# Optimization experiments

Hardware: AMD Instinct MI355X
Metric: run time of the kernel (lower is better)

Reference implementation:

```python
import jax, jax.numpy as jnp
import numpy as np

N, E = 10000, 160000
MUL0, MUL1, MUL2 = 64, 32, 16
DIM = MUL0 + MUL1 * 3 + MUL2 * 5          # 240
LAT, CPL, NTYPE = 128, 128, 95
NGATE = MUL1 + MUL2                        # 48 gate scalars
NCH = MUL0 + MUL1 + MUL2                   # 112 irrep channels
AVG_NEI = 16.0

# scaling_indices: per-channel index repeated over each irrep's dim
SCALE_IDX = np.concatenate([
    np.arange(MUL0),
    np.repeat(np.arange(MUL0, MUL0 + MUL1), 3),
    np.repeat(np.arange(MUL0 + MUL1, NCH), 5),
])


def _split(x, n):
    s = x[:, :MUL0]
    v1 = x[:, MUL0:MUL0 + MUL1 * 3].reshape(n, MUL1, 3)
    v2 = x[:, MUL0 + MUL1 * 3:].reshape(n, MUL2, 5)
    return s, v1, v2


def setup_inputs() -> dict:
    key = jax.random.key(0)
    ks = iter(jax.random.split(key, 48))
    rn = lambda *s: jax.random.normal(next(ks), s, dtype=jnp.float32)
    return dict(
        node_features=rn(N, DIM), edge_features=rn(E, DIM),
        latents=rn(E, LAT), msg_cpl=rn(N, CPL),
        node_onehot=jax.random.uniform(next(ks), (N, NTYPE), dtype=jnp.float32),
        wigner_D1=rn(E, 3, 3), wigner_D2=rn(E, 5, 5),
        so2_W0=rn(2 * MUL0, MUL0 + NGATE) * 0.08, so2_W1=rn(2 * MUL1, MUL1) * 0.12,
        so2_W2=rn(2 * MUL2, MUL2) * 0.17, so2_Ws=rn(LAT, NCH + NGATE) * 0.08,
        env_W=rn(LAT, NCH) * 0.08,
        post_W0=rn(MUL0, MUL0) * 0.12, post_b0=rn(MUL0) * 0.01,
        post_W1=rn(MUL1, MUL1) * 0.17, post_W2=rn(MUL2, MUL2) * 0.25,
        res_W0=rn(MUL0, MUL0) * 0.12, res_b0=rn(MUL0) * 0.01,
        res_W1=rn(MUL1, MUL1) * 0.17, res_W2=rn(MUL2, MUL2) * 0.25,
        cpl_W1=rn(CPL, CPL) * 0.08, cpl_b1=rn(CPL) * 0.01,
        cpl_W2=rn(CPL, NCH) * 0.08, cpl_b2=rn(NCH) * 0.01,
        gs_W=rn(MUL0, CPL) * 0.12, gs_b=rn(CPL) * 0.01,
        msg_W1=rn(2 * CPL, CPL) * 0.06, msg_b1=rn(CPL) * 0.01,
        msg_W2=rn(CPL, CPL) * 0.08, msg_b2=rn(CPL) * 0.01,
        ln_g=jnp.ones(CPL, jnp.float32), ln_b=jnp.zeros(CPL, jnp.float32),
        oh_w0=rn(MUL0, NTYPE) * 0.1, oh_w1=rn(MUL1, NTYPE) * 0.1, oh_w2=rn(MUL2, NTYPE) * 0.1,
        edge_index=jax.random.randint(next(ks), (2, E), 0, N),
    )


def _forward(node_features, edge_features, latents, msg_cpl, node_onehot,
             wigner_D1, wigner_D2, so2_W0, so2_W1, so2_W2, so2_Ws, env_W,
             post_W0, post_b0, post_W1, post_W2, res_W0, res_b0, res_W1, res_W2,
             cpl_W1, cpl_b1, cpl_W2, cpl_b2, gs_W, gs_b,
             msg_W1, msg_b1, msg_W2, msg_b2, ln_g, ln_b,
             oh_w0, oh_w1, oh_w2, edge_index):
    src = edge_index[0]
    ns, nv1, nv2 = _split(node_features, N)
    es, ev1, ev2 = _split(edge_features, E)
    # gather node feats to edges, concat with edge feats (per-l blocks)
    s_in = jnp.concatenate([ns[src], es], axis=1)                 # [E,128]
    v1_in = jnp.concatenate([nv1[src], ev1], axis=1)              # [E,64,3]
    v2_in = jnp.concatenate([nv2[src], ev2], axis=1)              # [E,32,5]
    # rotate into per-edge frame (Wigner D)
    v1_r = jnp.einsum('eij,ecj->eci', wigner_D1, v1_in)
    v2_r = jnp.einsum('eij,ecj->eci', wigner_D2, v2_in)
    # SO2 linear: shared channel mixing + latent-conditioned per-channel scales
    sc = latents @ so2_Ws                                         # [E,160]
    s_m = (s_in @ so2_W0) * sc[:, :MUL0 + NGATE]
    v1_m = jnp.einsum('eci,co->eoi', v1_r, so2_W1) * sc[:, MUL0 + NGATE:MUL0 + NGATE + MUL1, None]
    v2_m = jnp.einsum('eci,co->eoi', v2_r, so2_W2) * sc[:, MUL0 + NGATE + MUL1:, None]
    # rotate back
    v1_m = jnp.einsum('eji,eci->ecj', wigner_D1, v1_m)
    v2_m = jnp.einsum('eji,eci->ecj', wigner_D2, v2_m)
    # Gate activation
    s_act = jax.nn.silu(s_m[:, :MUL0])
    gates = jax.nn.sigmoid(s_m[:, MUL0:])
    v1_g = v1_m * gates[:, :MUL1, None]
    v2_g = v2_m * gates[:, MUL1:, None]
    # lin_post (per-l linear, bias on scalars)
    s_p = s_act @ post_W0 + post_b0
    v1_p = jnp.einsum('eci,co->eoi', v1_g, post_W1)
    v2_p = jnp.einsum('eci,co->eoi', v2_g, post_W2)
    # env element-wise weighting from latents
    w = latents @ env_W                                           # [E,112]
    s_p = s_p * w[:, :MUL0]
    v1_p = v1_p * w[:, MUL0:MUL0 + MUL1, None]
    v2_p = v2_p * w[:, MUL0 + MUL1:, None]
    msg = jnp.concatenate([s_p, v1_p.reshape(E, -1), v2_p.reshape(E, -1)], axis=1)
    # scatter-reduce to nodes + neighbor normalization
    agg = jax.ops.segment_sum(msg, src, num_segments=N) * (AVG_NEI ** -0.5)
    # coupling coefficients (per-channel, expanded by scaling_indices)
    coeffs = jax.nn.silu(msg_cpl @ cpl_W1 + cpl_b1) @ cpl_W2 + cpl_b2
    new_nf = agg * coeffs[:, SCALE_IDX]
    # coupling-channel update
    scal = new_nf[:, :MUL0] @ gs_W + gs_b
    h = jnp.concatenate([scal, msg_cpl], axis=1)
    upd = jax.nn.silu(h @ msg_W1 + msg_b1) @ msg_W2 + msg_b2
    mc = msg_cpl + upd
    mu = mc.mean(-1, keepdims=True)
    var = mc.var(-1, keepdims=True)
    msg_cpl_out = (mc - mu) * jax.lax.rsqrt(var + 1e-5) * ln_g + ln_b
    # residual mix with fixed logit-0 coefficients
    c = jax.nn.sigmoid(jnp.float32(0.0))
    c_old = jax.lax.rsqrt(c * c + 1.0)
    c_new = c * c_old
    rs = ns @ res_W0 + res_b0
    rv1 = jnp.einsum('eci,co->eoi', nv1, res_W1)
    rv2 = jnp.einsum('eci,co->eoi', nv2, res_W2)
    res = jnp.concatenate([rs, rv1.reshape(N, -1), rv2.reshape(N, -1)], axis=1)
    nf = c_new * new_nf + c_old * res
    # layer one-hot tensor product ('uvu' with 95x0e)
    inv = 1.0 / np.sqrt(NTYPE).astype(np.float32)
    g0 = (node_onehot @ oh_w0.T) * inv
    g1 = (node_onehot @ oh_w1.T) * inv
    g2 = (node_onehot @ oh_w2.T) * inv
    os_, ov1, ov2 = _split(nf, N)
    oh = jnp.concatenate([os_ * g0, (ov1 * g1[:, :, None]).reshape(N, -1),
                          (ov2 * g2[:, :, None]).reshape(N, -1)], axis=1)
    return nf + oh, msg_cpl_out


def reference(node_features, edge_features, latents, msg_cpl, node_onehot,
              wigner_D1, wigner_D2, so2_W0, so2_W1, so2_W2, so2_Ws, env_W,
              post_W0, post_b0, post_W1, post_W2, res_W0, res_b0, res_W1, res_W2,
              cpl_W1, cpl_b1, cpl_W2, cpl_b2, gs_W, gs_b,
              msg_W1, msg_b1, msg_W2, msg_b2, ln_g, ln_b,
              oh_w0, oh_w1, oh_w2, edge_index):
    return _forward(node_features, edge_features, latents, msg_cpl, node_onehot,
                    wigner_D1, wigner_D2, so2_W0, so2_W1, so2_W2, so2_Ws, env_W,
                    post_W0, post_b0, post_W1, post_W2, res_W0, res_b0, res_W1, res_W2,
                    cpl_W1, cpl_b1, cpl_W2, cpl_b2, gs_W, gs_b,
                    msg_W1, msg_b1, msg_W2, msg_b2, ln_g, ln_b,
                    oh_w0, oh_w1, oh_w2, edge_index)
```

## Files before the change

kernel.cpp:

```cpp
#include <hip/hip_runtime.h>

#define NN   10000
#define NE   160000
#define DIM  240
#define EB   16
#define NPB  16

typedef __bf16 bf16x8 __attribute__((ext_vector_type(8)));
typedef __bf16 bf16x4 __attribute__((ext_vector_type(4)));
typedef float  f32x4  __attribute__((ext_vector_type(4)));

__device__ __forceinline__ float sigf(float x) { return 1.0f / (1.0f + __expf(-x)); }

#define OFF_WB1 0
#define OFF_WB2 34816
#define OFF_W1  49152
#define OFF_W2  51200
#define OFF_PW0 51712
#define OFF_PW1 55808
#define OFF_PW2 56832
#define OHT_BYTE_OFF 131072
#define CNT_BYTE_OFF 196608
#define ROW_BYTE_OFF 237568
#define CUR_BYTE_OFF 282624
#define EID_BYTE_OFF 327680
#define MSG_BYTE_OFF 1048576

__global__ __launch_bounds__(256) void prep_kernel(
    const float* __restrict__ Ws, const float* __restrict__ We, const float* __restrict__ W0,
    const float* __restrict__ W1, const float* __restrict__ W2,
    const float* __restrict__ pW0, const float* __restrict__ pW1, const float* __restrict__ pW2,
    const float* __restrict__ w0g, const float* __restrict__ w1g, const float* __restrict__ w2g,
    __bf16* __restrict__ wsb, float* __restrict__ ohT)
{
    int tid = blockIdx.x * 256 + threadIdx.x;
    int stride = gridDim.x * 256;
    for (int idx = tid; idx < 17*4*512; idx += stride) {
        int j = idx & 7, lane = (idx >> 3) & 63, ks = (idx >> 9) & 3, nt = idx >> 11;
        int k = ks*32 + (lane >> 4)*8 + j, n = nt*16 + (lane & 15);
        float v = (n < 160) ? Ws[k*160 + n] : We[k*112 + (n - 160)];
        wsb[OFF_WB1 + idx] = (__bf16)v;
    }
    for (int idx = tid; idx < 7*4*512; idx += stride) {
        int j = idx & 7, lane = (idx >> 3) & 63, ks = (idx >> 9) & 3, nt = idx >> 11;
        int k = ks*32 + (lane >> 4)*8 + j, n = nt*16 + (lane & 15);
        wsb[OFF_WB2 + idx] = (__bf16)W0[k*112 + n];
    }
    for (int idx = tid; idx < 2*2*512; idx += stride) {
        int j = idx & 7, lane = (idx >> 3) & 63, ks = (idx >> 9) & 1, nt = idx >> 10;
        int k = ks*32 + (lane >> 4)*8 + j, n = nt*16 + (lane & 15);
        wsb[OFF_W1 + idx] = (__bf16)W1[k*32 + n];
    }
    for (int idx = tid; idx < 512; idx += stride) {
        int j = idx & 7, lane = (idx >> 3) & 63;
        int k = (lane >> 4)*8 + j, n = lane & 15;
        wsb[OFF_W2 + idx] = (__bf16)W2[k*16 + n];
    }
    for (int idx = tid; idx < 4*2*512; idx += stride) {
        int j = idx & 7, lane = (idx >> 3) & 63, ks = (idx >> 9) & 1, nt = idx >> 10;
        int k = ks*32 + (lane >> 4)*8 + j, n = nt*16 + (lane & 15);
        wsb[OFF_PW0 + idx] = (__bf16)pW0[k*64 + n];
    }
    for (int idx = tid; idx < 2*512; idx += stride) {
        int j = idx & 7, lane = (idx >> 3) & 63, nt = idx >> 9;
        int k = (lane >> 4)*8 + j, n = nt*16 + (lane & 15);
        wsb[OFF_PW1 + idx] = (__bf16)pW1[k*32 + n];
    }
    for (int idx = tid; idx < 512; idx += stride) {
        int j = idx & 7, lane = (idx >> 3) & 63;
        int k = (lane >> 4)*8 + j, n = lane & 15;
        wsb[OFF_PW2 + idx] = (k < 16) ? (__bf16)pW2[k*16 + n] : (__bf16)0.0f;
    }
    for (int idx = tid; idx < 96*112; idx += stride) {
        int k = idx / 112, n2 = idx - k*112;
        float v = 0.f;
        if (k < 95) {
            if (n2 < 64)      v = w0g[n2*95 + k];
            else if (n2 < 96) v = w1g[(n2-64)*95 + k];
            else              v = w2g[(n2-96)*95 + k];
        }
        ohT[idx] = v * 0.10259783521f;
    }
}

__global__ __launch_bounds__(256) void count_kernel(const int* __restrict__ src, int* __restrict__ cnt) {
    int e = blockIdx.x * 256 + threadIdx.x;
    if (e < NE) atomicAdd(&cnt[src[e]], 1);
}

__global__ __launch_bounds__(256) void scan_kernel(const int* __restrict__ cnt,
                                                   int* __restrict__ rowptr, int* __restrict__ cur) {
    __shared__ int part[256];
    int t = threadIdx.x;
    int base = t * 40;
    int local[40];
    int s = 0;
    #pragma unroll
    for (int i = 0; i < 40; i++) {
        int idx = base + i;
        int v = (idx < NN) ? cnt[idx] : 0;
        local[i] = s; s += v;
    }
    part[t] = s;
    __syncthreads();
    for (int off = 1; off < 256; off <<= 1) {
        int v = (t >= off) ? part[t - off] : 0;
        __syncthreads();
        part[t] += v;
        __syncthreads();
    }
    int pre = (t > 0) ? part[t - 1] : 0;
    #pragma unroll
    for (int i = 0; i < 40; i++) {
        int idx = base + i;
        if (idx < NN) { int r = pre + local[i]; rowptr[idx] = r; cur[idx] = r; }
    }
    if (t == 255) rowptr[NN] = part[255];
}

__global__ __launch_bounds__(256) void fill_kernel(const int* __restrict__ src,
                                                   int* __restrict__ cur, int* __restrict__ eidl) {
    int e = blockIdx.x * 256 + threadIdx.x;
    if (e < NE) {
        int slot = atomicAdd(&cur[src[e]], 1);
        eidl[slot] = e;
    }
}

__global__ __launch_bounds__(256) void agg_kernel(
    const __bf16* __restrict__ msg, const int* __restrict__ rowptr,
    const int* __restrict__ eidl, float* __restrict__ out0)
{
    int wid = threadIdx.x >> 6, lane = threadIdx.x & 63;
    int node = blockIdx.x * 4 + wid;
    if (node >= NN || lane >= 60) return;
    int beg = rowptr[node], end = rowptr[node + 1];
    float a0 = 0.f, a1 = 0.f, a2 = 0.f, a3 = 0.f;
    int i = beg;
    for (; i + 4 <= end; i += 4) {
        int e0 = eidl[i], e1 = eidl[i+1], e2 = eidl[i+2], e3 = eidl[i+3];
        bf16x4 v0 = *(const bf16x4*)(msg + (size_t)e0*240 + lane*4);
        bf16x4 v1 = *(const bf16x4*)(msg + (size_t)e1*240 + lane*4);
        bf16x4 v2 = *(const bf16x4*)(msg + (size_t)e2*240 + lane*4);
        bf16x4 v3 = *(const bf16x4*)(msg + (size_t)e3*240 + lane*4);
        a0 += (float)v0[0] + (float)v1[0] + (float)v2[0] + (float)v3[0];
        a1 += (float)v0[1] + (float)v1[1] + (float)v2[1] + (float)v3[1];
        a2 += (float)v0[2] + (float)v1[2] + (float)v2[2] + (float)v3[2];
        a3 += (float)v0[3] + (float)v1[3] + (float)v2[3] + (float)v3[3];
    }
    for (; i < end; i++) {
        int e = eidl[i];
        bf16x4 v = *(const bf16x4*)(msg + (size_t)e*240 + lane*4);
        a0 += (float)v[0]; a1 += (float)v[1]; a2 += (float)v[2]; a3 += (float)v[3];
    }
    float4 r = { a0, a1, a2, a3 };
    *(float4*)(out0 + (size_t)node*240 + lane*4) = r;
}

__global__ __launch_bounds__(256, 4) void edge_mfma_kernel(
    const float* __restrict__ nf, const float* __restrict__ ef,
    const float* __restrict__ latg, const float* __restrict__ D1g, const float* __restrict__ D2g,
    const float* __restrict__ pb0, const int* __restrict__ srcg,
    const __bf16* __restrict__ wsb, float* agg, __bf16* __restrict__ msgout)
{
    __shared__ __align__(16) unsigned char pool[37376];
    __bf16* Cb   = (__bf16*)(pool + 0);
    __bf16* vst  = (__bf16*)(pool + 0);
    __bf16* aLat = (__bf16*)(pool + 12544);
    __bf16* aSin = (__bf16*)(pool + 16640);
    __bf16* v1m  = (__bf16*)(pool + 12544);
    __bf16* v2m  = (__bf16*)(pool + 15712);
    __bf16* aV1r = (__bf16*)(pool + 20736);
    __bf16* aV2r = (__bf16*)(pool + 26880);
    __bf16* aSact= (__bf16*)(pool + 20736);
    __bf16* aV1g = (__bf16*)(pool + 22784);
    __bf16* aV2g = (__bf16*)(pool + 25856);
    float*  d1s  = (float*)(pool + 32000);
    float*  d2s  = (float*)(pool + 32576);
    float*  gts  = (float*)(pool + 34176);
    int*    srcs = (int*)  (pool + 37312);

    const int t    = threadIdx.x;
    const int wid  = t >> 6, lane = t & 63;
    const int e0   = blockIdx.x * EB;

    if (t < 16) srcs[t] = srcg[e0 + t];
    __syncthreads();

    for (int idx = t; idx < 144; idx += 256) d1s[idx] = D1g[e0*9  + idx];
    for (int idx = t; idx < 400; idx += 256) d2s[idx] = D2g[e0*25 + idx];
    for (int idx = t; idx < 16*88; idx += 256) {
        int e = idx / 88, c4 = idx - e*88;
        const float4* p = (c4 < 44) ? (const float4*)(nf + srcs[e]*240 + 64 + c4*4)
                                    : (const float4*)(ef + (e0 + e)*240 + 64 + (c4 - 44)*4);
        float4 f = *p;
        bf16x4 v = { (__bf16)f.x, (__bf16)f.y, (__bf16)f.z, (__bf16)f.w };
        *(bf16x4*)(vst + e*360 + c4*4) = v;
    }
    {
        int ks = t >> 6, l2 = t & 63, e = l2 & 15, q = l2 >> 4;
        int k0 = ks*32 + q*8;
        {
            const float4* p4 = (const float4*)(latg + (e0 + e)*128 + k0);
            float4 f0 = p4[0], f1 = p4[1];
            bf16x8 v;
            v[0]=(__bf16)f0.x; v[1]=(__bf16)f0.y; v[2]=(__bf16)f0.z; v[3]=(__bf16)f0.w;
            v[4]=(__bf16)f1.x; v[5]=(__bf16)f1.y; v[6]=(__bf16)f1.z; v[7]=(__bf16)f1.w;
            *(bf16x8*)(aLat + t*8) = v;
        }
        {
            const float* s2 = (k0 < 64) ? (nf + srcs[e]*240 + k0)
                                        : (ef + (e0 + e)*240 + (k0 - 64));
            const float4* p4 = (const float4*)s2;
            float4 f0 = p4[0], f1 = p4[1];
            bf16x8 v;
            v[0]=(__bf16)f0.x; v[1]=(__bf16)f0.y; v[2]=(__bf16)f0.z; v[3]=(__bf16)f0.w;
            v[4]=(__bf16)f1.x; v[5]=(__bf16)f1.y; v[6]=(__bf16)f1.z; v[7]=(__bf16)f1.w;
            *(bf16x8*)(aSin + t*8) = v;
        }
    }
    __syncthreads();

    for (int idx = t; idx < 384; idx += 256) {
        int i = idx >> 7, rem = idx & 127, ks = rem >> 6, l2 = rem & 63;
        int e = l2 & 15, q = l2 >> 4;
        int c0 = ks*32 + q*8;
        float da = d1s[e*9 + i*3 + 0], db = d1s[e*9 + i*3 + 1], dc = d1s[e*9 + i*3 + 2];
        const __bf16* ve = vst + e*360;
        bf16x8 v;
        #pragma unroll
        for (int j = 0; j < 8; j++) {
            int c = c0 + j;
            const __bf16* p = (c < 32) ? (ve + c*3) : (ve + 176 + (c - 32)*3);
            v[j] = (__bf16)(da*(float)p[0] + db*(float)p[1] + dc*(float)p[2]);
        }
        *(bf16x8*)(aV1r + idx*8) = v;
    }
    for (int idx = t; idx < 320; idx += 256) {
        int i = idx >> 6, l2 = idx & 63, e = l2 & 15, q = l2 >> 4;
        int c0 = q*8;
        const float* dd = d2s + e*25 + i*5;
        const __bf16* ve = vst + e*360;
        bf16x8 v;
        #pragma unroll
        for (int j = 0; j < 8; j++) {
            int c = c0 + j;
            const __bf16* p = (c < 16) ? (ve + 96 + c*5) : (ve + 272 + (c - 16)*5);
            float a = 0.f;
            #pragma unroll
            for (int z = 0; z < 5; z++) a += dd[z]*(float)p[z];
            v[j] = (__bf16)a;
        }
        *(bf16x8*)(aV2r + idx*8) = v;
    }
    __syncthreads();

    {
        int col16 = lane & 15, ebase = (lane >> 4)*4;
        bf16x8 aL[4], aS[4];
        #pragma unroll
        for (int ks = 0; ks < 4; ks++) {
            aL[ks] = *(const bf16x8*)(aLat + (ks*64 + lane)*8);
            aS[ks] = *(const bf16x8*)(aSin + (ks*64 + lane)*8);
        }
        #pragma unroll
        for (int it = 0; it < 6; it++) {
            int nt = wid + it*4;
            bool isLat = nt < 17;
            const __bf16* bB = isLat ? (wsb + OFF_WB1 + nt*2048)
                                     : (wsb + OFF_WB2 + (nt - 17)*2048);
            f32x4 acc = {0.f, 0.f, 0.f, 0.f};
            #pragma unroll
            for (int ks = 0; ks < 4; ks++) {
                bf16x8 b = *(const bf16x8*)(bB + (ks*64 + lane)*8);
                acc = __builtin_amdgcn_mfma_f32_16x16x32_bf16(isLat ? aL[ks] : aS[ks], b, acc, 0, 0, 0);
            }
            int col = (isLat ? nt*16 : 272 + (nt - 17)*16) + col16;
            #pragma unroll
            for (int r = 0; r < 4; r++) Cb[(ebase + r)*392 + col] = (__bf16)acc[r];
        }
    }
    __syncthreads();

    {
        int col16 = lane & 15, ebase = (lane >> 4)*4;
        for (int p = wid; p < 11; p += 4) {
            f32x4 acc = {0.f, 0.f, 0.f, 0.f};
            if (p < 6) {
                int i = p >> 1, nt = p & 1;
                #pragma unroll
                for (int ks = 0; ks < 2; ks++) {
                    bf16x8 a = *(const bf16x8*)(aV1r + ((i*2 + ks)*64 + lane)*8);
                    bf16x8 b = *(const bf16x8*)(wsb + OFF_W1 + ((nt*2 + ks)*64 + lane)*8);
                    acc = __builtin_amdgcn_mfma_f32_16x16x32_bf16(a, b, acc, 0, 0, 0);
                }
                int col = nt*16 + col16;
                #pragma unroll
                for (int r = 0; r < 4; r++) v1m[(i*16 + ebase + r)*33 + col] = (__bf16)acc[r];
            } else {
                int i = p - 6;
                bf16x8 a = *(const bf16x8*)(aV2r + (i*64 + lane)*8);
                bf16x8 b = *(const bf16x8*)(wsb + OFF_W2 + lane*8);
                acc = __builtin_amdgcn_mfma_f32_16x16x32_bf16(a, b, acc, 0, 0, 0);
                #pragma unroll
                for (int r = 0; r < 4; r++) v2m[(i*16 + ebase + r)*17 + col16] = (__bf16)acc[r];
            }
        }
    }
    __syncthreads();

    if (t < 128) {
        int ks = t >> 6, l2 = t & 63, e = l2 & 15, o0 = ks*32 + (l2 >> 4)*8;
        bf16x8 v;
        #pragma unroll
        for (int j = 0; j < 8; j++) {
            int o = o0 + j;
            float x = (float)Cb[e*392 + 272 + o] * (float)Cb[e*392 + o];
            v[j] = (__bf16)(x * sigf(x));
        }
        *(bf16x8*)(aSact + t*8) = v;
    }
    for (int idx = t; idx < 768; idx += 256) {
        int e = idx / 48, o = idx - e*48;
        float x = (float)Cb[e*392 + 336 + o] * (float)Cb[e*392 + 64 + o];
        gts[e*49 + o] = sigf(x);
    }
    __syncthreads();

    for (int idx = t; idx < 512; idx += 256) {
        if (idx < 192) {
            int i = idx >> 6, l2 = idx & 63, e = l2 & 15, c0 = (l2 >> 4)*8;
            float d0 = d1s[e*9 + i*3], d1 = d1s[e*9 + i*3 + 1], d2 = d1s[e*9 + i*3 + 2];
            bf16x8 v;
            #pragma unroll
            for (int j = 0; j < 8; j++) {
                int c = c0 + j;
                float scl = (float)Cb[e*392 + 112 + c];
                float g   = gts[e*49 + c];
                float m0 = (float)v1m[e*33 + c], m1 = (float)v1m[(16 + e)*33 + c],
                      m2 = (float)v1m[(32 + e)*33 + c];
                v[j] = (__bf16)(g * scl * (d0*m0 + d1*m1 + d2*m2));
            }
            *(bf16x8*)(aV1g + idx*8) = v;
        } else {
            int idx2 = idx - 192;
            int i = idx2 >> 6, l2 = idx2 & 63, e = l2 & 15, c0 = (l2 >> 4)*8;
            const float* dd = d2s + e*25 + i*5;
            bf16x8 v;
            #pragma unroll
            for (int j = 0; j < 8; j++) {
                int c = c0 + j;
                float val = 0.f;
                if (c < 16) {
                    float scl = (float)Cb[e*392 + 144 + c];
                    float g   = gts[e*49 + 32 + c];
                    float acc = 0.f;
                    #pragma unroll
                    for (int z = 0; z < 5; z++) acc += dd[z] * (float)v2m[(z*16 + e)*17 + c];
                    val = g * scl * acc;
                }
                v[j] = (__bf16)val;
            }
            *(bf16x8*)(aV2g + idx2*8) = v;
        }
    }
    __syncthreads();

    {
        int col16 = lane & 15, ebase = (lane >> 4)*4;
        for (int p = wid; p < 15; p += 4) {
            f32x4 acc = {0.f, 0.f, 0.f, 0.f};
            if (p < 4) {
                int nt = p;
                #pragma unroll
                for (int ks = 0; ks < 2; ks++) {
                    bf16x8 a = *(const bf16x8*)(aSact + (ks*64 + lane)*8);
                    bf16x8 b = *(const bf16x8*)(wsb + OFF_PW0 + ((nt*2 + ks)*64 + lane)*8);
                    acc = __builtin_amdgcn_mfma_f32_16x16x32_bf16(a, b, acc, 0, 0, 0);
                }
                int o = nt*16 + col16;
                float bias = pb0[o];
                #pragma unroll
                for (int r = 0; r < 4; r++) {
                    int e = ebase + r;
                    float val = (acc[r] + bias) * (float)Cb[e*392 + 160 + o];
                    if (msgout) msgout[(size_t)(e0 + e)*240 + o] = (__bf16)val;
                    else        atomicAdd(agg + srcs[e]*240 + o, val);
                }
            } else if (p < 10) {
                int q = p - 4, i = q >> 1, nt = q & 1;
                bf16x8 a = *(const bf16x8*)(aV1g + (i*64 + lane)*8);
                bf16x8 b = *(const bf16x8*)(wsb + OFF_PW1 + (nt*64 + lane)*8);
                acc = __builtin_amdgcn_mfma_f32_16x16x32_bf16(a, b, acc, 0, 0, 0);
                int o = nt*16 + col16;
                #pragma unroll
                for (int r = 0; r < 4; r++) {
                    int e = ebase + r;
                    float val = acc[r] * (float)Cb[e*392 + 224 + o];
                    if (msgout) msgout[(size_t)(e0 + e)*240 + 64 + o*3 + i] = (__bf16)val;
                    else        atomicAdd(agg + srcs[e]*240 + 64 + o*3 + i, val);
                }
            } else {
                int i = p - 10;
                bf16x8 a = *(const bf16x8*)(aV2g + (i*64 + lane)*8);
                bf16x8 b = *(const bf16x8*)(wsb + OFF_PW2 + lane*8);
                acc = __builtin_amdgcn_mfma_f32_16x16x32_bf16(a, b, acc, 0, 0, 0);
                #pragma unroll
                for (int r = 0; r < 4; r++) {
                    int e = ebase + r;
                    float val = acc[r] * (float)Cb[e*392 + 256 + col16];
                    if (msgout) msgout[(size_t)(e0 + e)*240 + 160 + col16*5 + i] = (__bf16)val;
                    else        atomicAdd(agg + srcs[e]*240 + 160 + col16*5 + i, val);
                }
            }
        }
    }
}

__global__ __launch_bounds__(256, 2) void node_kernel(
    const float* __restrict__ nf, const float* __restrict__ mcplg,
    const float* __restrict__ ohg,
    const float* __restrict__ cW1, const float* __restrict__ cb1,
    const float* __restrict__ cW2, const float* __restrict__ cb2,
    const float* __restrict__ gsW, const float* __restrict__ gsb,
    const float* __restrict__ mW1, const float* __restrict__ mb1,
    const float* __restrict__ mW2, const float* __restrict__ mb2,
    const float* __restrict__ lng, const float* __restrict__ lnb,
    const float* __restrict__ rW0, const float* __restrict__ rb0,
    const float* __restrict__ rW1, const float* __restrict__ rW2,
    const float* __restrict__ ohT, float* out0, float* out1)
{
    __shared__ __align__(16) unsigned char pool[68608];
    float* mcp  = (float*)(pool + 0);
    float* ohv  = (float*)(pool + 8192);
    float* nsr  = (float*)(pool + 14336);
    float* anew = (float*)(pool + 29696);
    float* t12  = (float*)(pool + 45056);
    float* cfg  = (float*)(pool + 53248);
    float* scm  = (float*)(pool + 60416);

    const int t  = threadIdx.x;
    const int g  = t >> 7;
    const int o  = t & 127;
    const int nb = g * 8;
    const int n0 = blockIdx.x * NPB;

    for (int idx = t; idx < NPB * 128; idx += 256) {
        int n = idx >> 7, k = idx & 127;
        mcp[n*128 + k] = mcplg[(n0 + n) * 128 + k];
    }
    for (int idx = t; idx < NPB * 96; idx += 256) {
        int n = idx / 96, k = idx - n * 96;
        ohv[n*96 + k] = (k < 95) ? ohg[(n0 + n) * 95 + k] : 0.f;
    }
    for (int idx = t; idx < NPB * 240; idx += 256) {
        int n = idx / 240, k = idx - n * 240;
        nsr[n*240 + k]  = nf[(n0 + n) * DIM + k];
        anew[n*240 + k] = out0[(n0 + n) * DIM + k];
    }
    __syncthreads();

    {
        float a[8]; float b = cb1[o];
        #pragma unroll
        for (int i = 0; i < 8; i++) a[i] = b;
        #pragma unroll 2
        for (int k4 = 0; k4 < 32; k4++) {
            float w0 = cW1[(4*k4+0)*128 + o], w1 = cW1[(4*k4+1)*128 + o],
                  w2 = cW1[(4*k4+2)*128 + o], w3 = cW1[(4*k4+3)*128 + o];
            #pragma unroll
            for (int i = 0; i < 8; i++) {
                float4 m = *(const float4*)&mcp[(nb+i)*128 + 4*k4];
                a[i] += m.x*w0 + m.y*w1 + m.z*w2 + m.w*w3;
            }
        }
        #pragma unroll
        for (int i = 0; i < 8; i++) { float x = a[i]; t12[(nb+i)*128 + o] = x * sigf(x); }
    }
    __syncthreads();

    if (o < 112) {
        float a[8]; float b = cb2[o];
        #pragma unroll
        for (int i = 0; i < 8; i++) a[i] = b;
        #pragma unroll 2
        for (int k4 = 0; k4 < 32; k4++) {
            float w0 = cW2[(4*k4+0)*112 + o], w1 = cW2[(4*k4+1)*112 + o],
                  w2 = cW2[(4*k4+2)*112 + o], w3 = cW2[(4*k4+3)*112 + o];
            #pragma unroll
            for (int i = 0; i < 8; i++) {
                float4 m = *(const float4*)&t12[(nb+i)*128 + 4*k4];
                a[i] += m.x*w0 + m.y*w1 + m.z*w2 + m.w*w3;
            }
        }
        #pragma unroll
        for (int i = 0; i < 8; i++) cfg[(nb+i)*112 + o] = a[i];
    }
    __syncthreads();

    for (int idx = t; idx < NPB * 240; idx += 256) {
        int n = idx / 240, d = idx - n * 240;
        int ch = (d < 64) ? d : (d < 160 ? 64 + (d - 64) / 3 : 96 + (d - 160) / 5);
        anew[n*240 + d] *= 0.25f * cfg[n*112 + ch];
    }
    __syncthreads();

    {
        float a[8]; float b = gsb[o];
        #pragma unroll
        for (int i = 0; i < 8; i++) a[i] = b;
        #pragma unroll 2
        for (int k4 = 0; k4 < 16; k4++) {
            float w0 = gsW[(4*k4+0)*128 + o], w1 = gsW[(4*k4+1)*128 + o],
                  w2 = gsW[(4*k4+2)*128 + o], w3 = gsW[(4*k4+3)*128 + o];
            #pragma unroll
            for (int i = 0; i < 8; i++) {
                float4 m = *(const float4*)&anew[(nb+i)*240 + 4*k4];
                a[i] += m.x*w0 + m.y*w1 + m.z*w2 + m.w*w3;
            }
        }
        #pragma unroll
        for (int i = 0; i < 8; i++) scm[(nb+i)*128 + o] = a[i];
    }
    __syncthreads();

    {
        float a[8]; float b = mb1[o];
        #pragma unroll
        for (int i = 0; i < 8; i++) a[i] = b;
        #pragma unroll 2
        for (int k4 = 0; k4 < 32; k4++) {
            float w0 = mW1[(4*k4+0)*128 + o], w1 = mW1[(4*k4+1)*128 + o],
                  w2 = mW1[(4*k4+2)*128 + o], w3 = mW1[(4*k4+3)*128 + o];
            #pragma unroll
            for (int i = 0; i < 8; i++) {
                float4 m = *(const float4*)&scm[(nb+i)*128 + 4*k4];
                a[i] += m.x*w0 + m.y*w1 + m.z*w2 + m.w*w3;
            }
        }
        #pragma unroll 2
        for (int k4 = 0; k4 < 32; k4++) {
            float w0 = mW1[(128+4*k4+0)*128 + o], w1 = mW1[(128+4*k4+1)*128 + o],
                  w2 = mW1[(128+4*k4+2)*128 + o], w3 = mW1[(128+4*k4+3)*128 + o];
            #pragma unroll
            for (int i = 0; i < 8; i++) {
                float4 m = *(const float4*)&mcp[(nb+i)*128 + 4*k4];
                a[i] += m.x*w0 + m.y*w1 + m.z*w2 + m.w*w3;
            }
        }
        #pragma unroll
        for (int i = 0; i < 8; i++) { float x = a[i]; t12[(nb+i)*128 + o] = x * sigf(x); }
    }
    __syncthreads();

    {
        float a[8]; float b = mb2[o];
        #pragma unroll
        for (int i = 0; i < 8; i++) a[i] = b;
        #pragma unroll 2
        for (int k4 = 0; k4 < 32; k4++) {
            float w0 = mW2[(4*k4+0)*128 + o], w1 = mW2[(4*k4+1)*128 + o],
                  w2 = mW2[(4*k4+2)*128 + o], w3 = mW2[(4*k4+3)*128 + o];
            #pragma unroll
            for (int i = 0; i < 8; i++) {
                float4 m = *(const float4*)&t12[(nb+i)*128 + 4*k4];
                a[i] += m.x*w0 + m.y*w1 + m.z*w2 + m.w*w3;
            }
        }
        #pragma unroll
        for (int i = 0; i < 8; i++) scm[(nb+i)*128 + o] = mcp[(nb+i)*128 + o] + a[i];
    }
    __syncthreads();

    {
        int n = t >> 4, l = t & 15;
        float x[8]; float s = 0.f, ss = 0.f;
        #pragma unroll
        for (int i = 0; i < 8; i++) { x[i] = scm[n*128 + l + 16*i]; s += x[i]; ss += x[i]*x[i]; }
        #pragma unroll
        for (int off = 8; off > 0; off >>= 1) {
            s  += __shfl_down(s,  off, 16);
            ss += __shfl_down(ss, off, 16);
        }
        s  = __shfl(s, 0, 16);
        ss = __shfl(ss, 0, 16);
        float mu   = s * (1.f / 128.f);
        float var  = ss * (1.f / 128.f) - mu * mu;
        float rstd = rsqrtf(var + 1e-5f);
        float* op = out1 + (n0 + n) * 128;
        #pragma unroll
        for (int i = 0; i < 8; i++) {
            int c = l + 16*i;
            op[c] = (x[i] - mu) * rstd * lng[c] + lnb[c];
        }
    }

    if (o < 112) {
        float a[8] = {0.f,0.f,0.f,0.f,0.f,0.f,0.f,0.f};
        #pragma unroll 2
        for (int k4 = 0; k4 < 24; k4++) {
            float w0 = ohT[(4*k4+0)*112 + o], w1 = ohT[(4*k4+1)*112 + o],
                  w2 = ohT[(4*k4+2)*112 + o], w3 = ohT[(4*k4+3)*112 + o];
            #pragma unroll
            for (int i = 0; i < 8; i++) {
                float4 m = *(const float4*)&ohv[(nb+i)*96 + 4*k4];
                a[i] += m.x*w0 + m.y*w1 + m.z*w2 + m.w*w3;
            }
        }
        #pragma unroll
        for (int i = 0; i < 8; i++) cfg[(nb+i)*112 + o] = a[i];
    }
    __syncthreads();

    const float c_new = 0.4472135955f;
    const float c_old = 0.8944271910f;
    for (int idx = t; idx < NPB * 240; idx += 256) {
        int n = idx / 240, d = idx - n * 240;
        float res, gg;
        if (d < 64) {
            float acc = rb0[d];
            #pragma unroll 4
            for (int c = 0; c < 64; c++) acc += nsr[n*240 + c] * rW0[c * 64 + d];
            res = acc; gg = cfg[n*112 + d];
        } else if (d < 160) {
            int dd = d - 64, oo = dd / 3, j = dd - oo * 3;
            float acc = 0.f;
            #pragma unroll 4
            for (int c = 0; c < 32; c++) acc += nsr[n*240 + 64 + c*3 + j] * rW1[c * 32 + oo];
            res = acc; gg = cfg[n*112 + 64 + oo];
        } else {
            int dd = d - 160, oo = dd / 5, j = dd - oo * 5;
            float acc = 0.f;
            #pragma unroll 4
            for (int c = 0; c < 16; c++) acc += nsr[n*240 + 160 + c*5 + j] * rW2[c * 16 + oo];
            res = acc; gg = cfg[n*112 + 96 + oo];
        }
        float v = c_new * anew[n*240 + d] + c_old * res;
        out0[(n0 + n) * DIM + d] = v * (1.f + gg);
    }
}

extern "C" void kernel_launch(void* const* d_in, const int* in_sizes, int n_in,
                              void* d_out, int out_size, void* d_ws, size_t ws_size,
                              hipStream_t stream) {
    const float* nf      = (const float*)d_in[0];
    const float* ef      = (const float*)d_in[1];
    const float* lat     = (const float*)d_in[2];
    const float* mcpl    = (const float*)d_in[3];
    const float* ohot    = (const float*)d_in[4];
    const float* D1      = (const float*)d_in[5];
    const float* D2      = (const float*)d_in[6];
    const float* so2_W0  = (const float*)d_in[7];
    const float* so2_W1  = (const float*)d_in[8];
    const float* so2_W2  = (const float*)d_in[9];
    const float* so2_Ws  = (const float*)d_in[10];
    const float* env_W   = (const float*)d_in[11];
    const float* post_W0 = (const float*)d_in[12];
    const float* post_b0 = (const float*)d_in[13];
    const float* post_W1 = (const float*)d_in[14];
    const float* post_W2 = (const float*)d_in[15];
    const float* res_W0  = (const float*)d_in[16];
    const float* res_b0  = (const float*)d_in[17];
    const float* res_W1  = (const float*)d_in[18];
    const float* res_W2  = (const float*)d_in[19];
    const float* cpl_W1  = (const float*)d_in[20];
    const float* cpl_b1  = (const float*)d_in[21];
    const float* cpl_W2  = (const float*)d_in[22];
    const float* cpl_b2  = (const float*)d_in[23];
    const float* gs_W    = (const float*)d_in[24];
    const float* gs_b    = (const float*)d_in[25];
    const float* msg_W1  = (const float*)d_in[26];
    const float* msg_b1  = (const float*)d_in[27];
    const float* msg_W2  = (const float*)d_in[28];
    const float* msg_b2  = (const float*)d_in[29];
    const float* ln_g    = (const float*)d_in[30];
    const float* ln_b    = (const float*)d_in[31];
    const float* oh_w0   = (const float*)d_in[32];
    const float* oh_w1   = (const float*)d_in[33];
    const float* oh_w2   = (const float*)d_in[34];
    const int*   eidx    = (const int*)d_in[35];

    float* out0 = (float*)d_out;
    float* out1 = (float*)d_out + (size_t)NN * DIM;
    char*   wsB = (char*)d_ws;
    __bf16* wsb = (__bf16*)d_ws;
    float*  ohT = (float*)(wsB + OHT_BYTE_OFF);

    const size_t need = (size_t)MSG_BYTE_OFF + (size_t)NE * 240 * 2;
    const bool planA = ws_size >= need;

    (void)hipMemsetAsync(out0, 0, (size_t)NN * DIM * sizeof(float), stream);

    prep_kernel<<<56, 256, 0, stream>>>(so2_Ws, env_W, so2_W0, so2_W1, so2_W2,
                                        post_W0, post_W1, post_W2,
                                        oh_w0, oh_w1, oh_w2, wsb, ohT);

    if (planA) {
        int*    cnt  = (int*)(wsB + CNT_BYTE_OFF);
        int*    row  = (int*)(wsB + ROW_BYTE_OFF);
        int*    cur  = (int*)(wsB + CUR_BYTE_OFF);
        int*    eidl = (int*)(wsB + EID_BYTE_OFF);
        __bf16* msg  = (__bf16*)(wsB + MSG_BYTE_OFF);

        (void)hipMemsetAsync(cnt, 0, 10240 * sizeof(int), stream);
        count_kernel<<<(NE + 255) / 256, 256, 0, stream>>>(eidx, cnt);
        scan_kernel<<<1, 256, 0, stream>>>(cnt, row, cur);
        fill_kernel<<<(NE + 255) / 256, 256, 0, stream>>>(eidx, cur, eidl);

        edge_mfma_kernel<<<NE / EB, 256, 0, stream>>>(
            nf, ef, lat, D1, D2, post_b0, eidx, wsb, out0, msg);

        agg_kernel<<<(NN + 3) / 4, 256, 0, stream>>>(msg, row, eidl, out0);
    } else {
        edge_mfma_kernel<<<NE / EB, 256, 0, stream>>>(
            nf, ef, lat, D1, D2, post_b0, eidx, wsb, out0, nullptr);
    }

    node_kernel<<<NN / NPB, 256, 0, stream>>>(
        nf, mcpl, ohot, cpl_W1, cpl_b1, cpl_W2, cpl_b2, gs_W, gs_b,
        msg_W1, msg_b1, msg_W2, msg_b2, ln_g, ln_b,
        res_W0, res_b0, res_W1, res_W2, ohT, out0, out1);
}
```

Before: 749.6 us.

## Fold forward and inverse Wigner rotations into precomputed D·D products

Drops the separate rotate-into-frame pass over the l=1/l=2 features. The SO(2) matmuls now read features directly from transposed LDS tiles, and the back-rotation uses precomputed per-edge D·D products (e1s/e2s) in place of D itself. This removes one LDS staging pass and two barriers, and the srcs preload barrier is replaced by direct global index reads. It only matches the original if rotating before the channel-mixing matmul commutes with it, which holds because the mixing is linear per component. It also changes where bf16 rounding happens and relies on padded LDS strides (40 and 24) to avoid bank conflicts.

```diff
diff --git a/kernel.cpp b/kernel.cpp
--- a/kernel.cpp
+++ b/kernel.cpp
@@ -163,45 +163,68 @@
     const float* __restrict__ pb0, const int* __restrict__ srcg,
     const __bf16* __restrict__ wsb, float* agg, __bf16* __restrict__ msgout)
 {
-    __shared__ __align__(16) unsigned char pool[37376];
+    __shared__ __align__(16) unsigned char pool[39936];
     __bf16* Cb   = (__bf16*)(pool + 0);
-    __bf16* vst  = (__bf16*)(pool + 0);
     __bf16* aLat = (__bf16*)(pool + 12544);
     __bf16* aSin = (__bf16*)(pool + 16640);
     __bf16* v1m  = (__bf16*)(pool + 12544);
-    __bf16* v2m  = (__bf16*)(pool + 15712);
-    __bf16* aV1r = (__bf16*)(pool + 20736);
-    __bf16* aV2r = (__bf16*)(pool + 26880);
-    __bf16* aSact= (__bf16*)(pool + 20736);
-    __bf16* aV1g = (__bf16*)(pool + 22784);
-    __bf16* aV2g = (__bf16*)(pool + 25856);
-    float*  d1s  = (float*)(pool + 32000);
-    float*  d2s  = (float*)(pool + 32576);
-    float*  gts  = (float*)(pool + 34176);
-    int*    srcs = (int*)  (pool + 37312);
+    __bf16* v2m  = (__bf16*)(pool + 16384);
+    __bf16* vt1  = (__bf16*)(pool + 20736);
+    __bf16* vt2  = (__bf16*)(pool + 27136);
+    __bf16* aV1g = (__bf16*)(pool + 20736);
+    __bf16* aV2g = (__bf16*)(pool + 23808);
+    float*  d1s  = (float*)(pool + 32512);
+    float*  d2s  = (float*)(pool + 33088);
+    float*  gts  = (float*)(pool + 32512);
+    __bf16* aSact= (__bf16*)(pool + 35648);
+    float*  e1s  = (float*)(pool + 37696);
+    float*  e2s  = (float*)(pool + 38272);
 
     const int t    = threadIdx.x;
     const int wid  = t >> 6, lane = t & 63;
     const int e0   = blockIdx.x * EB;
 
-    if (t < 16) srcs[t] = srcg[e0 + t];
-    __syncthreads();
-
     for (int idx = t; idx < 144; idx += 256) d1s[idx] = D1g[e0*9  + idx];
     for (int idx = t; idx < 400; idx += 256) d2s[idx] = D2g[e0*25 + idx];
-    for (int idx = t; idx < 16*88; idx += 256) {
-        int e = idx / 88, c4 = idx - e*88;
-        const float4* p = (c4 < 44) ? (const float4*)(nf + srcs[e]*240 + 64 + c4*4)
-                                    : (const float4*)(ef + (e0 + e)*240 + 64 + (c4 - 44)*4);
-        float4 f = *p;
-        bf16x4 v = { (__bf16)f.x, (__bf16)f.y, (__bf16)f.z, (__bf16)f.w };
-        *(bf16x4*)(vst + e*360 + c4*4) = v;
-    }
-    {
-        int ks = t >> 6, l2 = t & 63, e = l2 & 15, q = l2 >> 4;
-        int k0 = ks*32 + q*8;
+    {
+        int e = t >> 4, half = (t >> 3) & 1, cq = t & 7;
+        const float* base = half ? (ef + (size_t)(e0 + e)*240 + 64 + cq*12)
+                                 : (nf + (size_t)srcg[e0 + e]*240 + 64 + cq*12);
+        float4 f0 = *(const float4*)base;
+        float4 f1 = *(const float4*)(base + 4);
+        float4 f2 = *(const float4*)(base + 8);
+        float f[12] = {f0.x,f0.y,f0.z,f0.w,f1.x,f1.y,f1.z,f1.w,f2.x,f2.y,f2.z,f2.w};
+        int c = half*32 + cq*4;
+        __bf16* dst = vt1 + e*200 + c;
+        #pragma unroll
+        for (int i = 0; i < 3; i++) {
+            bf16x4 v = {(__bf16)f[i], (__bf16)f[3+i], (__bf16)f[6+i], (__bf16)f[9+i]};
+            *(bf16x4*)(dst + i*64) = v;
+        }
+    }
+    if (t < 128) {
+        int e = t >> 3, half = (t >> 2) & 1, cq = t & 3;
+        const float* base = half ? (ef + (size_t)(e0 + e)*240 + 160 + cq*20)
+                                 : (nf + (size_t)srcg[e0 + e]*240 + 160 + cq*20);
+        float f[20];
+        #pragma unroll
+        for (int k = 0; k < 5; k++) {
+            float4 q4 = *(const float4*)(base + k*4);
+            f[4*k] = q4.x; f[4*k+1] = q4.y; f[4*k+2] = q4.z; f[4*k+3] = q4.w;
+        }
+        int c = half*16 + cq*4;
+        __bf16* dst = vt2 + e*168 + c;
+        #pragma unroll
+        for (int z = 0; z < 5; z++) {
+            bf16x4 v = {(__bf16)f[z], (__bf16)f[5+z], (__bf16)f[10+z], (__bf16)f[15+z]};
+            *(bf16x4*)(dst + z*32) = v;
+        }
+    }
+    {
+        int ks = t >> 6, l2 = t & 63, e = l2 & 15;
+        int k0 = ks*32 + (l2 >> 4)*8;
         {
-            const float4* p4 = (const float4*)(latg + (e0 + e)*128 + k0);
+            const float4* p4 = (const float4*)(latg + (size_t)(e0 + e)*128 + k0);
             float4 f0 = p4[0], f1 = p4[1];
             bf16x8 v;
             v[0]=(__bf16)f0.x; v[1]=(__bf16)f0.y; v[2]=(__bf16)f0.z; v[3]=(__bf16)f0.w;
@@ -209,8 +232,8 @@
             *(bf16x8*)(aLat + t*8) = v;
         }
         {
-            const float* s2 = (k0 < 64) ? (nf + srcs[e]*240 + k0)
-                                        : (ef + (e0 + e)*240 + (k0 - 64));
+            const float* s2 = (k0 < 64) ? (nf + (size_t)srcg[e0 + e]*240 + k0)
+                                        : (ef + (size_t)(e0 + e)*240 + (k0 - 64));
             const float4* p4 = (const float4*)s2;
             float4 f0 = p4[0], f1 = p4[1];
             bf16x8 v;
@@ -221,40 +244,6 @@
     }
     __syncthreads();
 
-    for (int idx = t; idx < 384; idx += 256) {
-        int i = idx >> 7, rem = idx & 127, ks = rem >> 6, l2 = rem & 63;
-        int e = l2 & 15, q = l2 >> 4;
-        int c0 = ks*32 + q*8;
-        float da = d1s[e*9 + i*3 + 0], db = d1s[e*9 + i*3 + 1], dc = d1s[e*9 + i*3 + 2];
-        const __bf16* ve = vst + e*360;
-        bf16x8 v;
-        #pragma unroll
-        for (int j = 0; j < 8; j++) {
-            int c = c0 + j;
-            const __bf16* p = (c < 32) ? (ve + c*3) : (ve + 176 + (c - 32)*3);
-            v[j] = (__bf16)(da*(float)p[0] + db*(float)p[1] + dc*(float)p[2]);
-        }
-        *(bf16x8*)(aV1r + idx*8) = v;
-    }
-    for (int idx = t; idx < 320; idx += 256) {
-        int i = idx >> 6, l2 = idx & 63, e = l2 & 15, q = l2 >> 4;
-        int c0 = q*8;
-        const float* dd = d2s + e*25 + i*5;
-        const __bf16* ve = vst + e*360;
-        bf16x8 v;
-        #pragma unroll
-        for (int j = 0; j < 8; j++) {
-            int c = c0 + j;
-            const __bf16* p = (c < 16) ? (ve + 96 + c*5) : (ve + 272 + (c - 16)*5);
-            float a = 0.f;
-            #pragma unroll
-            for (int z = 0; z < 5; z++) a += dd[z]*(float)p[z];
-            v[j] = (__bf16)a;
-        }
-        *(bf16x8*)(aV2r + idx*8) = v;
-    }
-    __syncthreads();
-
     {
         int col16 = lane & 15, ebase = (lane >> 4)*4;
         bf16x8 aL[4], aS[4];
@@ -280,35 +269,48 @@
             for (int r = 0; r < 4; r++) Cb[(ebase + r)*392 + col] = (__bf16)acc[r];
         }
     }
-    __syncthreads();
-
-    {
-        int col16 = lane & 15, ebase = (lane >> 4)*4;
+    for (int idx = t; idx < 544; idx += 256) {
+        if (idx < 144) {
+            int e = idx / 9, r = idx - e*9, i = r / 3, k = r - i*3;
+            const float* d = d1s + e*9;
+            e1s[idx] = d[i*3+0]*d[0*3+k] + d[i*3+1]*d[1*3+k] + d[i*3+2]*d[2*3+k];
+        } else {
+            int j = idx - 144;
+            int e = j / 25, r = j - e*25, i = r / 5, k = r - i*5;
+            const float* d = d2s + e*25;
+            float a = 0.f;
+            #pragma unroll
+            for (int tt = 0; tt < 5; tt++) a += d[i*5+tt] * d[tt*5+k];
+            e2s[j] = a;
+        }
+    }
+    __syncthreads();
+
+    {
+        int col16 = lane & 15, er = lane & 15, q8 = (lane >> 4)*8, ebase = (lane >> 4)*4;
         for (int p = wid; p < 11; p += 4) {
             f32x4 acc = {0.f, 0.f, 0.f, 0.f};
             if (p < 6) {
                 int i = p >> 1, nt = p & 1;
                 #pragma unroll
                 for (int ks = 0; ks < 2; ks++) {
-                    bf16x8 a = *(const bf16x8*)(aV1r + ((i*2 + ks)*64 + lane)*8);
+                    bf16x8 a = *(const bf16x8*)(vt1 + er*200 + i*64 + ks*32 + q8);
                     bf16x8 b = *(const bf16x8*)(wsb + OFF_W1 + ((nt*2 + ks)*64 + lane)*8);
                     acc = __builtin_amdgcn_mfma_f32_16x16x32_bf16(a, b, acc, 0, 0, 0);
                 }
                 int col = nt*16 + col16;
                 #pragma unroll
-                for (int r = 0; r < 4; r++) v1m[(i*16 + ebase + r)*33 + col] = (__bf16)acc[r];
+                for (int r = 0; r < 4; r++) v1m[(i*16 + ebase + r)*40 + col] = (__bf16)acc[r];
             } else {
                 int i = p - 6;
-                bf16x8 a = *(const bf16x8*)(aV2r + (i*64 + lane)*8);
+                bf16x8 a = *(const bf16x8*)(vt2 + er*168 + i*32 + q8);
                 bf16x8 b = *(const bf16x8*)(wsb + OFF_W2 + lane*8);
                 acc = __builtin_amdgcn_mfma_f32_16x16x32_bf16(a, b, acc, 0, 0, 0);
                 #pragma unroll
-                for (int r = 0; r < 4; r++) v2m[(i*16 + ebase + r)*17 + col16] = (__bf16)acc[r];
-            }
-        }
-    }
-    __syncthreads();
-
+                for (int r = 0; r < 4; r++) v2m[(i*16 + ebase + r)*24 + col16] = (__bf16)acc[r];
+            }
+        }
+    }
     if (t < 128) {
         int ks = t >> 6, l2 = t & 63, e = l2 & 15, o0 = ks*32 + (l2 >> 4)*8;
         bf16x8 v;
@@ -330,36 +332,42 @@
     for (int idx = t; idx < 512; idx += 256) {
         if (idx < 192) {
             int i = idx >> 6, l2 = idx & 63, e = l2 & 15, c0 = (l2 >> 4)*8;
-            float d0 = d1s[e*9 + i*3], d1 = d1s[e*9 + i*3 + 1], d2 = d1s[e*9 + i*3 + 2];
+            float z0 = e1s[e*9 + i*3], z1 = e1s[e*9 + i*3 + 1], z2 = e1s[e*9 + i*3 + 2];
+            bf16x8 m0 = *(const bf16x8*)(v1m + (0*16 + e)*40 + c0);
+            bf16x8 m1 = *(const bf16x8*)(v1m + (1*16 + e)*40 + c0);
+            bf16x8 m2 = *(const bf16x8*)(v1m + (2*16 + e)*40 + c0);
+            bf16x8 s8 = *(const bf16x8*)(Cb + e*392 + 112 + c0);
             bf16x8 v;
             #pragma unroll
             for (int j = 0; j < 8; j++) {
-                int c = c0 + j;
-                float scl = (float)Cb[e*392 + 112 + c];
-                float g   = gts[e*49 + c];
-                float m0 = (float)v1m[e*33 + c], m1 = (float)v1m[(16 + e)*33 + c],
-                      m2 = (float)v1m[(32 + e)*33 + c];
-                v[j] = (__bf16)(g * scl * (d0*m0 + d1*m1 + d2*m2));
+                float g = gts[e*49 + c0 + j];
+                float a = z0*(float)m0[j] + z1*(float)m1[j] + z2*(float)m2[j];
+                v[j] = (__bf16)(g * (float)s8[j] * a);
             }
             *(bf16x8*)(aV1g + idx*8) = v;
         } else {
             int idx2 = idx - 192;
             int i = idx2 >> 6, l2 = idx2 & 63, e = l2 & 15, c0 = (l2 >> 4)*8;
-            const float* dd = d2s + e*25 + i*5;
             bf16x8 v;
-            #pragma unroll
-            for (int j = 0; j < 8; j++) {
-                int c = c0 + j;
-                float val = 0.f;
-                if (c < 16) {
-                    float scl = (float)Cb[e*392 + 144 + c];
-                    float g   = gts[e*49 + 32 + c];
-                    float acc = 0.f;
-                    #pragma unroll
-                    for (int z = 0; z < 5; z++) acc += dd[z] * (float)v2m[(z*16 + e)*17 + c];
-                    val = g * scl * acc;
+            if (c0 < 16) {
+                const float* ee = e2s + e*25 + i*5;
+                float z0 = ee[0], z1 = ee[1], z2 = ee[2], z3 = ee[3], z4 = ee[4];
+                bf16x8 m0 = *(const bf16x8*)(v2m + (0*16 + e)*24 + c0);
+                bf16x8 m1 = *(const bf16x8*)(v2m + (1*16 + e)*24 + c0);
+                bf16x8 m2 = *(const bf16x8*)(v2m + (2*16 + e)*24 + c0);
+                bf16x8 m3 = *(const bf16x8*)(v2m + (3*16 + e)*24 + c0);
+                bf16x8 m4 = *(const bf16x8*)(v2m + (4*16 + e)*24 + c0);
+                bf16x8 s8 = *(const bf16x8*)(Cb + e*392 + 144 + c0);
+                #pragma unroll
+                for (int j = 0; j < 8; j++) {
+                    float g = gts[e*49 + 32 + c0 + j];
+                    float a = z0*(float)m0[j] + z1*(float)m1[j] + z2*(float)m2[j]
+                            + z3*(float)m3[j] + z4*(float)m4[j];
+                    v[j] = (__bf16)(g * (float)s8[j] * a);
                 }
-                v[j] = (__bf16)val;
+            } else {
+                #pragma unroll
+                for (int j = 0; j < 8; j++) v[j] = (__bf16)0.0f;
             }
             *(bf16x8*)(aV2g + idx2*8) = v;
         }
@@ -385,7 +393,7 @@
                     int e = ebase + r;
                     float val = (acc[r] + bias) * (float)Cb[e*392 + 160 + o];
                     if (msgout) msgout[(size_t)(e0 + e)*240 + o] = (__bf16)val;
-                    else        atomicAdd(agg + srcs[e]*240 + o, val);
+                    else        atomicAdd(agg + (size_t)srcg[e0 + e]*240 + o, val);
                 }
             } else if (p < 10) {
                 int q = p - 4, i = q >> 1, nt = q & 1;
@@ -398,7 +406,7 @@
                     int e = ebase + r;
                     float val = acc[r] * (float)Cb[e*392 + 224 + o];
                     if (msgout) msgout[(size_t)(e0 + e)*240 + 64 + o*3 + i] = (__bf16)val;
-                    else        atomicAdd(agg + srcs[e]*240 + 64 + o*3 + i, val);
+                    else        atomicAdd(agg + (size_t)srcg[e0 + e]*240 + 64 + o*3 + i, val);
                 }
             } else {
                 int i = p - 10;
@@ -410,7 +418,7 @@
                     int e = ebase + r;
                     float val = acc[r] * (float)Cb[e*392 + 256 + col16];
                     if (msgout) msgout[(size_t)(e0 + e)*240 + 160 + col16*5 + i] = (__bf16)val;
-                    else        atomicAdd(agg + srcs[e]*240 + 160 + col16*5 + i, val);
+                    else        atomicAdd(agg + (size_t)srcg[e0 + e]*240 + 160 + col16*5 + i, val);
                 }
             }
         }
```

New measurement: 699.6 us. -6.7%, faster.
